# Performance work log

Measured on AMD Instinct MI355X. Metric: run time of the kernel, lower is better.

Reference implementation:

```python
import jax, jax.numpy as jnp
import numpy as np

N = 2048        # nodes
IN_DIM = 128    # input feature dim
K = 8           # channels
D = 32          # per-channel dim (C_dim)
ITERS = 4       # routing iterations
BETA = 1.0      # attention temperature
EPS = 1e-12     # F.normalize eps


def l2norm(x):
    # F.normalize(x, dim=-1): x / max(||x||_2, eps)
    n = jnp.linalg.norm(x, axis=-1, keepdims=True)
    return x / jnp.maximum(n, EPS)


def setup_inputs() -> dict:
    key = jax.random.key(0)
    k1, k2, k3, k4 = jax.random.split(key, 4)
    adj = jax.random.randint(k1, (N, N), 0, 2, dtype=jnp.int32)
    features = jax.random.normal(k2, (N, IN_DIM), dtype=jnp.float32)
    # parameters initialized ~ N(0,1) as in init_parameters
    W = jax.random.normal(k3, (K, IN_DIM, D), dtype=jnp.float32)
    b = jax.random.normal(k4, (K, D), dtype=jnp.float32)
    return {"adj": adj, "features": features, "W": W, "b": b}


def reference(adj, features, W, b):
    mask = (adj > 0)[None, :, :]                         # [1, N, N]
    # per-channel projection + row L2 normalize -> Z: [K, N, D]
    Z = l2norm(jnp.einsum('nd,kdc->knc', features, W) + b[:, None, :])
    for _ in range(ITERS):
        # per-channel masked attention scores [K, N, N]
        att = jnp.einsum('knc,kmc->knm', Z, Z)
        att = jnp.where(mask, att, 0.0) / BETA
        # softmax across channels (dim=2 in torch after cat == K axis here)
        att = jax.nn.softmax(att, axis=0)
        att = jnp.where(mask, att, 0.0)
        # weighted aggregate + residual + L2 normalize
        Z = l2norm(Z + jnp.einsum('knm,kmc->knc', att, Z))
    # concat channels along feature dim -> [N, K*D]
    return jnp.transpose(Z, (1, 0, 2)).reshape(N, K * D)
```

## Files before the change

### kernel.cpp

```cpp
#include <hip/hip_runtime.h>
#include <hip/hip_bf16.h>
#include <hip/hip_fp16.h>

#define NN 2048
#define KK 8
#define DD 32
#define ZSZ (KK * NN * DD)
#define ZS2 (KK * NN * 16)
#define PSTR 20

typedef __attribute__((ext_vector_type(8))) short short8;
typedef __attribute__((ext_vector_type(4))) float f32x4;
typedef __attribute__((ext_vector_type(4))) unsigned int u32x4;

union UU { u32x4 q; short8 v; unsigned int u[4]; };

#define SELHI 0x07060302u
#define SELLO 0x05040100u

__device__ __forceinline__ unsigned int prm(unsigned int a, unsigned int b, unsigned int sel) {
  return __builtin_amdgcn_perm(a, b, sel);
}
__device__ __forceinline__ unsigned int bfr(float x) {
  unsigned int u = __float_as_uint(x);
  return (u + 0x7fffu + ((u >> 16) & 1u)) >> 16;
}
__device__ __forceinline__ unsigned int packp(float a, float b) {
  union { __hip_bfloat162 h; unsigned int u; } cv;
  cv.h = __float22bfloat162_rn(make_float2(a, b));
  return cv.u;
}
__device__ __forceinline__ unsigned int packh(float a, float b) {
  union { __half2 h; unsigned int u; } cv;
  cv.h = __float22half2_rn(make_float2(a, b));
  return cv.u;
}
__device__ __forceinline__ float2 unpackh(unsigned int u) {
  union { unsigned int u; __half2 h; } cv;
  cv.u = u;
  return __half22float2(cv.h);
}
__device__ __forceinline__ f32x4 MF(short8 a, short8 b, f32x4 c) {
  return __builtin_amdgcn_mfma_f32_16x16x32_bf16(a, b, c, 0, 0, 0);
}
__device__ __forceinline__ short8 as_s8(u32x4 x) { UU u; u.q = x; return u.v; }

__global__ __launch_bounds__(256) void pm_kernel(const float* __restrict__ feat,
                                                 const float* __restrict__ W,
                                                 const float* __restrict__ bias,
                                                 float* __restrict__ Z,
                                                 unsigned short* __restrict__ Zghi,
                                                 unsigned short* __restrict__ Zthi,
                                                 const int* __restrict__ adj,
                                                 unsigned int* __restrict__ mbits) {
  const int t = threadIdx.x;
  if (blockIdx.x < 256) {
    const int nb = blockIdx.x * 8;
    const int k = t >> 5, c = t & 31;
    float s[8];
#pragma unroll
    for (int j = 0; j < 8; ++j) s[j] = bias[k * DD + c];
    const float* w = W + (k * 128) * DD + c;
    const float* fp = feat + nb * 128;
#pragma unroll 4
    for (int d = 0; d < 128; ++d) {
      float wv = w[d * DD];
#pragma unroll
      for (int j = 0; j < 8; ++j) s[j] = fmaf(fp[j * 128 + d], wv, s[j]);
    }
    unsigned int hi[8];
#pragma unroll
    for (int j = 0; j < 8; ++j) {
      float sq = s[j] * s[j];
#pragma unroll
      for (int off = 16; off > 0; off >>= 1) sq += __shfl_xor(sq, off, 32);
      float z = s[j] / fmaxf(sqrtf(sq), 1e-12f);
      Z[(k * NN + nb + j) * DD + c] = z;
      hi[j] = bfr(z);
      Zghi[(k * NN + nb + j) * DD + c] = (unsigned short)hi[j];
    }
    uint4 tp = make_uint4(hi[0] | (hi[1] << 16), hi[2] | (hi[3] << 16),
                          hi[4] | (hi[5] << 16), hi[6] | (hi[7] << 16));
    *(uint4*)&Zthi[(size_t)k * DD * NN + (size_t)c * NN + nb] = tp;
  } else {
    const int base = (blockIdx.x - 256) * 1024 + t;
    const int lane = t & 63;
    int v[4];
#pragma unroll
    for (int rr = 0; rr < 4; ++rr) v[rr] = adj[base + 256 * rr];
#pragma unroll
    for (int rr = 0; rr < 4; ++rr) {
      int idx = base + 256 * rr;
      unsigned long long b = __ballot(v[rr] > 0);
      if (lane == 0) mbits[idx >> 5] = (unsigned int)b;
      if (lane == 32) mbits[idx >> 5] = (unsigned int)(b >> 32);
    }
  }
}

template <int NCt>
__global__ __launch_bounds__(256) void rp_kernel(const float* __restrict__ Zin,
                                                 const unsigned int* __restrict__ partU,
                                                 float* __restrict__ Zout,
                                                 unsigned short* __restrict__ Zghi,
                                                 unsigned short* __restrict__ Zthi) {
  __shared__ unsigned short T[DD][33];
  const int t = threadIdx.x;
  const int k = blockIdx.x >> 6, mt = blockIdx.x & 63;
  const int m0 = mt * 32;
  const int mloc = t >> 3, c4 = t & 7;
  const size_t idx = (size_t)(k * NN + m0 + mloc) * DD + 4 * c4;
  float4 v = *(const float4*)&Zin[idx];
#pragma unroll
  for (int j = 0; j < NCt; ++j) {
    uint2 pp = *(const uint2*)&partU[(size_t)j * ZS2 + (size_t)(k * NN + m0 + mloc) * 16 + 2 * c4];
    float2 f0 = unpackh(pp.x), f1 = unpackh(pp.y);
    v.x += f0.x; v.y += f0.y; v.z += f1.x; v.w += f1.y;
  }
  float sq = v.x * v.x + v.y * v.y + v.z * v.z + v.w * v.w;
  sq += __shfl_xor(sq, 1, 8);
  sq += __shfl_xor(sq, 2, 8);
  sq += __shfl_xor(sq, 4, 8);
  const float sc = 1.0f / fmaxf(sqrtf(sq), 1e-12f);
  float z[4] = {v.x * sc, v.y * sc, v.z * sc, v.w * sc};
  *(float4*)&Zout[idx] = make_float4(z[0], z[1], z[2], z[3]);
  unsigned int hi[4];
#pragma unroll
  for (int e = 0; e < 4; ++e) {
    hi[e] = bfr(z[e]);
    T[4 * c4 + e][mloc] = (unsigned short)hi[e];
  }
  *(uint2*)&Zghi[idx] = make_uint2(hi[0] | (hi[1] << 16), hi[2] | (hi[3] << 16));
  __syncthreads();
  const int cloc = t >> 3, m4 = t & 7;
  unsigned int o0 = (unsigned int)T[cloc][4 * m4 + 0] | ((unsigned int)T[cloc][4 * m4 + 1] << 16);
  unsigned int o1 = (unsigned int)T[cloc][4 * m4 + 2] | ((unsigned int)T[cloc][4 * m4 + 3] << 16);
  *(uint2*)&Zthi[(size_t)k * DD * NN + (size_t)cloc * NN + m0 + 4 * m4] = make_uint2(o0, o1);
}

template <int NS>
__global__ __launch_bounds__(256, 2) void iter_kernel(const unsigned short* __restrict__ Zghi,
                                                      const unsigned short* __restrict__ Zthi,
                                                      const unsigned int* __restrict__ mbits,
                                                      unsigned int* __restrict__ partU) {
  __shared__ __align__(16) unsigned int lds[8192 + 4 * 4 * 16 * PSTR];
  const int t = threadIdx.x;
  const int w = t >> 6;
  const int lane = t & 63;
  const int l15 = lane & 15;
  const int g = lane >> 4;
  const int nw = blockIdx.x * 64 + w * 16;
  const int mchunk = blockIdx.y * (NS * 32);

  const unsigned int* Zg = (const unsigned int*)Zghi;
  const unsigned int* Zt = (const unsigned int*)Zthi;

  short8 A[KK];
#pragma unroll
  for (int k = 0; k < KK; ++k)
    A[k] = as_s8(*(const u32x4*)&Zg[(size_t)(k * NN + nw + l15) * 16 + 4 * g]);

  unsigned int mwa[4][NS];
#pragma unroll
  for (int r = 0; r < 4; ++r)
#pragma unroll
    for (int q4 = 0; q4 < NS / 4; ++q4) {
      uint4 m4 = *(const uint4*)&mbits[(size_t)(nw + 4 * g + r) * 64 + (mchunk >> 5) + 4 * q4];
      mwa[r][4 * q4 + 0] = m4.x; mwa[r][4 * q4 + 1] = m4.y;
      mwa[r][4 * q4 + 2] = m4.z; mwa[r][4 * q4 + 3] = m4.w;
    }

  f32x4 O[KK][2];
#pragma unroll
  for (int k = 0; k < KK; ++k)
#pragma unroll
    for (int ch = 0; ch < 2; ++ch) O[k][ch] = {0.0f, 0.0f, 0.0f, 0.0f};

  const int sqd = t & 3;
  const int sr0 = t >> 2;

  u32x4 Lgh[4], Lth[4];
  auto do_loads = [&](int mb) {
#pragma unroll
    for (int j = 0; j < 4; ++j) {
      int r = 64 * j + sr0;
      int k = r >> 5, rm = r & 31;
      Lgh[j] = *(const u32x4*)&Zg[(size_t)k * (NN * 16) + (size_t)(mb + rm) * 16 + sqd * 4];
      Lth[j] = *(const u32x4*)&Zt[(size_t)k * (NN * 16) + (size_t)rm * (NN / 2) + (mb >> 1) + sqd * 4];
    }
  };
  do_loads(mchunk);

  unsigned int* Pw = &lds[8192 + w * (4 * 16 * PSTR)];

#pragma unroll
  for (int st = 0; st < NS; ++st) {
    const int mb = mchunk + st * 32;
    __syncthreads();
#pragma unroll
    for (int j = 0; j < 4; ++j) {
      int r = 64 * j + sr0;
      *(u32x4*)&lds[r * 16 + 4 * sqd] = Lgh[j];
      *(u32x4*)&lds[4096 + r * 16 + 4 * sqd] = Lth[j];
    }
    __syncthreads();
    if (st + 1 < NS) do_loads(mb + 32);

#pragma unroll
    for (int sub = 0; sub < 2; ++sub) {
      f32x4 S[KK];
#pragma unroll
      for (int k = 0; k < KK; ++k) {
        int m = 16 * sub + l15;
        u32x4 bh = *(const u32x4*)&lds[(k * 32 + m) * 16 + 4 * g];
        f32x4 z = {0.0f, 0.0f, 0.0f, 0.0f};
        S[k] = MF(A[k], as_s8(bh), z);
      }
#pragma unroll
      for (int r = 0; r < 4; ++r) {
        float e[KK];
        float sum = 0.0f;
#pragma unroll
        for (int k = 0; k < KK; ++k) { e[k] = __expf(S[k][r]); sum += e[k]; }
        int ml = 16 * sub + l15;
        float f = ((mwa[r][st] >> ml) & 1u) ? __builtin_amdgcn_rcpf(sum) : 0.0f;
#pragma unroll
        for (int k = 0; k < KK; ++k) S[k][r] = e[k] * f;
      }
#pragma unroll
      for (int kp = 0; kp < 4; ++kp)
#pragma unroll
        for (int r = 0; r < 4; ++r) {
          int n = 4 * g + r;
          Pw[kp * (16 * PSTR) + n * PSTR + 16 * sub + l15] =
              packp(S[2 * kp][r], S[2 * kp + 1][r]);
        }
    }

#pragma unroll
    for (int kp = 0; kp < 4; ++kp) {
      const unsigned int* Pr = &Pw[kp * (16 * PSTR) + l15 * PSTR + 8 * g];
      u32x4 a0 = *(const u32x4*)Pr;
      u32x4 a1 = *(const u32x4*)(Pr + 4);
      UU pk0, pk1;
      pk0.u[0] = prm(a0.y, a0.x, SELLO); pk0.u[1] = prm(a0.w, a0.z, SELLO);
      pk0.u[2] = prm(a1.y, a1.x, SELLO); pk0.u[3] = prm(a1.w, a1.z, SELLO);
      pk1.u[0] = prm(a0.y, a0.x, SELHI); pk1.u[1] = prm(a0.w, a0.z, SELHI);
      pk1.u[2] = prm(a1.y, a1.x, SELHI); pk1.u[3] = prm(a1.w, a1.z, SELHI);
#pragma unroll
      for (int kk = 0; kk < 2; ++kk) {
        int k = 2 * kp + kk;
#pragma unroll
        for (int ch = 0; ch < 2; ++ch) {
          int c = 16 * ch + l15;
          u32x4 b = *(const u32x4*)&lds[4096 + (k * 32 + c) * 16 + 4 * g];
          O[k][ch] = MF(kk ? pk1.v : pk0.v, as_s8(b), O[k][ch]);
        }
      }
    }
  }

  unsigned int* dst = partU + (size_t)blockIdx.y * ZS2;
  const int even = ((l15 & 1) == 0);
#pragma unroll
  for (int k = 0; k < KK; ++k)
#pragma unroll
    for (int ch = 0; ch < 2; ++ch) {
      f32x4 o = O[k][ch];
#pragma unroll
      for (int r = 0; r < 4; ++r) {
        float partner = __shfl_xor(o[r], 1);
        if (even) {
          dst[(size_t)(k * NN + nw + 4 * g + r) * 16 + ((16 * ch + l15) >> 1)] =
              packh(o[r], partner);
        }
      }
    }
}

template <int NCt>
__global__ __launch_bounds__(256) void ro_kernel(const float* __restrict__ Zin,
                                                 const unsigned int* __restrict__ partU,
                                                 float* __restrict__ out) {
  const int n = blockIdx.x, t = threadIdx.x;
  const int k = t >> 5, c = t & 31;
  float v = Zin[(size_t)(k * NN + n) * DD + c];
#pragma unroll
  for (int j = 0; j < NCt; ++j) {
    unsigned int pu = partU[(size_t)j * ZS2 + (size_t)(k * NN + n) * 16 + (c >> 1)];
    float2 f = unpackh(pu);
    v += (c & 1) ? f.y : f.x;
  }
  float sq = v * v;
#pragma unroll
  for (int off = 16; off > 0; off >>= 1) sq += __shfl_xor(sq, off, 32);
  out[n * (KK * DD) + t] = v / fmaxf(sqrtf(sq), 1e-12f);
}

extern "C" void kernel_launch(void* const* d_in, const int* in_sizes, int n_in,
                              void* d_out, int out_size, void* d_ws, size_t ws_size,
                              hipStream_t stream) {
  const int* adj = (const int*)d_in[0];
  const float* feat = (const float*)d_in[1];
  const float* W = (const float*)d_in[2];
  const float* b = (const float*)d_in[3];
  float* out = (float*)d_out;

  int NC = 16;
  while (NC > 4) {
    size_t need = ((size_t)ZSZ * 2 + NN * 64) * 4 + (size_t)ZSZ * 2 * 2 + (size_t)NC * ZS2 * 4;
    if (need <= ws_size) break;
    NC >>= 1;
  }

  float* Z0 = (float*)d_ws;
  float* Z1 = Z0 + ZSZ;
  unsigned short* Zghi = (unsigned short*)(Z1 + ZSZ);
  unsigned short* Zthi = Zghi + ZSZ;
  unsigned int* mbits = (unsigned int*)(Zthi + ZSZ);
  unsigned int* partU = mbits + NN * 64;

  pm_kernel<<<256 + 4096, 256, 0, stream>>>(feat, W, b, Z0, Zghi, Zthi, adj, mbits);

  float* zi = Z0;
  float* zo = Z1;
  for (int it = 0; it < 4; ++it) {
    if (NC == 16)
      iter_kernel<4><<<dim3(32, 16), 256, 0, stream>>>(Zghi, Zthi, mbits, partU);
    else if (NC == 8)
      iter_kernel<8><<<dim3(32, 8), 256, 0, stream>>>(Zghi, Zthi, mbits, partU);
    else
      iter_kernel<16><<<dim3(32, 4), 256, 0, stream>>>(Zghi, Zthi, mbits, partU);
    if (it < 3) {
      if (NC == 16)
        rp_kernel<16><<<512, 256, 0, stream>>>(zi, partU, zo, Zghi, Zthi);
      else if (NC == 8)
        rp_kernel<8><<<512, 256, 0, stream>>>(zi, partU, zo, Zghi, Zthi);
      else
        rp_kernel<4><<<512, 256, 0, stream>>>(zi, partU, zo, Zghi, Zthi);
      float* tmp = zi; zi = zo; zo = tmp;
    } else {
      if (NC == 16)
        ro_kernel<16><<<NN, 256, 0, stream>>>(zi, partU, out);
      else if (NC == 8)
        ro_kernel<8><<<NN, 256, 0, stream>>>(zi, partU, out);
      else
        ro_kernel<4><<<NN, 256, 0, stream>>>(zi, partU, out);
    }
  }
}
```

Baseline: 201.9 us.

## Split node chunks finer, shrink P staging LDS, raise occupancy to four blocks

The m dimension is now split into 32 chunks of 64 columns (NS=2), giving 1024 blocks instead of 512 and more partial sums for the reduce kernels to combine. The per-wave P staging buffer in LDS is cut to a single kp slice that is rewritten before each kp's MFMA. The packed values are held in registers between those rewrites. Launch bounds are raised to 4 blocks per CU. The workspace-size fallback is removed, so the doubled partial buffer must fit the workspace, and the reduce step reads twice as many partials.

```diff
diff --git a/kernel.cpp b/kernel.cpp
--- a/kernel.cpp
+++ b/kernel.cpp
@@ -8,6 +8,7 @@
 #define ZSZ (KK * NN * DD)
 #define ZS2 (KK * NN * 16)
 #define PSTR 20
+#define NCH 32
 
 typedef __attribute__((ext_vector_type(8))) short short8;
 typedef __attribute__((ext_vector_type(4))) float f32x4;
@@ -139,11 +140,11 @@
 }
 
 template <int NS>
-__global__ __launch_bounds__(256, 2) void iter_kernel(const unsigned short* __restrict__ Zghi,
+__global__ __launch_bounds__(256, 4) void iter_kernel(const unsigned short* __restrict__ Zghi,
                                                       const unsigned short* __restrict__ Zthi,
                                                       const unsigned int* __restrict__ mbits,
                                                       unsigned int* __restrict__ partU) {
-  __shared__ __align__(16) unsigned int lds[8192 + 4 * 4 * 16 * PSTR];
+  __shared__ __align__(16) unsigned int lds[8192 + 4 * 16 * PSTR];
   const int t = threadIdx.x;
   const int w = t >> 6;
   const int lane = t & 63;
@@ -164,11 +165,8 @@
 #pragma unroll
   for (int r = 0; r < 4; ++r)
 #pragma unroll
-    for (int q4 = 0; q4 < NS / 4; ++q4) {
-      uint4 m4 = *(const uint4*)&mbits[(size_t)(nw + 4 * g + r) * 64 + (mchunk >> 5) + 4 * q4];
-      mwa[r][4 * q4 + 0] = m4.x; mwa[r][4 * q4 + 1] = m4.y;
-      mwa[r][4 * q4 + 2] = m4.z; mwa[r][4 * q4 + 3] = m4.w;
-    }
+    for (int wi = 0; wi < NS; ++wi)
+      mwa[r][wi] = mbits[(size_t)(nw + 4 * g + r) * 64 + (mchunk >> 5) + wi];
 
   f32x4 O[KK][2];
 #pragma unroll
@@ -191,7 +189,7 @@
   };
   do_loads(mchunk);
 
-  unsigned int* Pw = &lds[8192 + w * (4 * 16 * PSTR)];
+  unsigned int* Pw = &lds[8192 + w * (16 * PSTR)];
 
 #pragma unroll
   for (int st = 0; st < NS; ++st) {
@@ -206,6 +204,7 @@
     __syncthreads();
     if (st + 1 < NS) do_loads(mb + 32);
 
+    unsigned int pp[4][2][4];
 #pragma unroll
     for (int sub = 0; sub < 2; ++sub) {
       f32x4 S[KK];
@@ -226,20 +225,21 @@
         float f = ((mwa[r][st] >> ml) & 1u) ? __builtin_amdgcn_rcpf(sum) : 0.0f;
 #pragma unroll
         for (int k = 0; k < KK; ++k) S[k][r] = e[k] * f;
+#pragma unroll
+        for (int kp = 0; kp < 4; ++kp)
+          pp[kp][sub][r] = packp(S[2 * kp][r], S[2 * kp + 1][r]);
       }
-#pragma unroll
-      for (int kp = 0; kp < 4; ++kp)
-#pragma unroll
-        for (int r = 0; r < 4; ++r) {
-          int n = 4 * g + r;
-          Pw[kp * (16 * PSTR) + n * PSTR + 16 * sub + l15] =
-              packp(S[2 * kp][r], S[2 * kp + 1][r]);
-        }
     }
 
 #pragma unroll
     for (int kp = 0; kp < 4; ++kp) {
-      const unsigned int* Pr = &Pw[kp * (16 * PSTR) + l15 * PSTR + 8 * g];
+#pragma unroll
+      for (int sub = 0; sub < 2; ++sub)
+#pragma unroll
+        for (int r = 0; r < 4; ++r)
+          Pw[(4 * g + r) * PSTR + 16 * sub + l15] = pp[kp][sub][r];
+
+      const unsigned int* Pr = &Pw[l15 * PSTR + 8 * g];
       u32x4 a0 = *(const u32x4*)Pr;
       u32x4 a1 = *(const u32x4*)(Pr + 4);
       UU pk0, pk1;
@@ -306,13 +306,6 @@
   const float* b = (const float*)d_in[3];
   float* out = (float*)d_out;
 
-  int NC = 16;
-  while (NC > 4) {
-    size_t need = ((size_t)ZSZ * 2 + NN * 64) * 4 + (size_t)ZSZ * 2 * 2 + (size_t)NC * ZS2 * 4;
-    if (need <= ws_size) break;
-    NC >>= 1;
-  }
-
   float* Z0 = (float*)d_ws;
   float* Z1 = Z0 + ZSZ;
   unsigned short* Zghi = (unsigned short*)(Z1 + ZSZ);
@@ -325,27 +318,12 @@
   float* zi = Z0;
   float* zo = Z1;
   for (int it = 0; it < 4; ++it) {
-    if (NC == 16)
-      iter_kernel<4><<<dim3(32, 16), 256, 0, stream>>>(Zghi, Zthi, mbits, partU);
-    else if (NC == 8)
-      iter_kernel<8><<<dim3(32, 8), 256, 0, stream>>>(Zghi, Zthi, mbits, partU);
-    else
-      iter_kernel<16><<<dim3(32, 4), 256, 0, stream>>>(Zghi, Zthi, mbits, partU);
+    iter_kernel<2><<<dim3(32, NCH), 256, 0, stream>>>(Zghi, Zthi, mbits, partU);
     if (it < 3) {
-      if (NC == 16)
-        rp_kernel<16><<<512, 256, 0, stream>>>(zi, partU, zo, Zghi, Zthi);
-      else if (NC == 8)
-        rp_kernel<8><<<512, 256, 0, stream>>>(zi, partU, zo, Zghi, Zthi);
-      else
-        rp_kernel<4><<<512, 256, 0, stream>>>(zi, partU, zo, Zghi, Zthi);
+      rp_kernel<NCH><<<512, 256, 0, stream>>>(zi, partU, zo, Zghi, Zthi);
       float* tmp = zi; zi = zo; zo = tmp;
     } else {
-      if (NC == 16)
-        ro_kernel<16><<<NN, 256, 0, stream>>>(zi, partU, out);
-      else if (NC == 8)
-        ro_kernel<8><<<NN, 256, 0, stream>>>(zi, partU, out);
-      else
-        ro_kernel<4><<<NN, 256, 0, stream>>>(zi, partU, out);
-    }
-  }
-}
+      ro_kernel<NCH><<<NN, 256, 0, stream>>>(zi, partU, out);
+    }
+  }
+}
```

Measured after the change: 261.0 us. +29.3%, slower.
